# Optimization experiments

Measured on AMD Instinct MI355X. Metric: run time of the kernel, lower is better.

The kernel has to match this reference:

```python
import jax, jax.numpy as jnp
import numpy as np

B, S, D, H = 4, 2048, 1024, 16
DEPTH = D // H


def setup_inputs() -> dict:
    key = jax.random.key(0)
    ks = jax.random.split(key, 12)
    inp = {
        "Q": jax.random.normal(ks[0], (B, S, D), jnp.float32),
        "K": jax.random.normal(ks[1], (B, S, D), jnp.float32),
        "V": jax.random.normal(ks[2], (B, S, D), jnp.float32),
        "mask": jax.random.randint(ks[3], (B, 1, S, S), 0, 2, jnp.int32),
        "Wq": jax.random.normal(ks[4], (D, D), jnp.float32) / np.sqrt(D),
        "bq": jnp.zeros((D,), jnp.float32),
        "Wk": jax.random.normal(ks[5], (D, D), jnp.float32) / np.sqrt(D),
        "bk": jnp.zeros((D,), jnp.float32),
        "Wv": jax.random.normal(ks[6], (D, D), jnp.float32) / np.sqrt(D),
        "bv": jnp.zeros((D,), jnp.float32),
        "Wo": jax.random.normal(ks[7], (D, D), jnp.float32) / np.sqrt(D),
        "bo": jnp.zeros((D,), jnp.float32),
    }
    return inp


def _split_heads(x):
    # (B, S, D) -> (B, H, S, depth)
    b, s, _ = x.shape
    return x.reshape(b, s, H, DEPTH).transpose(0, 2, 1, 3)


def reference(Q, K, V, mask, Wq, bq, Wk, bk, Wv, bv, Wo, bo):
    q = _split_heads(Q @ Wq + bq)  # (B,H,S,d)
    k = _split_heads(K @ Wk + bk)
    v = _split_heads(V @ Wv + bv)
    scores = jnp.einsum("bhqd,bhkd->bhqk", q, k) / jnp.sqrt(jnp.float32(DEPTH))
    m = mask.astype(jnp.bool_).astype(jnp.float32)  # (B,1,S,S)
    scores = scores + (1.0 - m) * -1e9
    attn = jax.nn.softmax(scores, axis=-1)  # (B,H,S,S)
    ctx = jnp.einsum("bhqk,bhkd->bhqd", attn, v)
    ctx = ctx.transpose(0, 2, 1, 3).reshape(Q.shape[0], -1, D)  # (B,S,D)
    out = ctx @ Wo + bo
    return out, attn
```

## Files before the change

kernel.cpp:

```cpp
#include <hip/hip_runtime.h>
#include <hip/hip_bf16.h>

#define B_ 4
#define S_ 2048
#define D_ 1024
#define H_ 16
#define TSZ 8388608L

typedef short short8 __attribute__((ext_vector_type(8)));
typedef float f32x4 __attribute__((ext_vector_type(4)));

__device__ inline unsigned short f2b(float f) {
  __hip_bfloat16 h = __float2bfloat16(f);
  return __builtin_bit_cast(unsigned short, h);
}
__device__ inline void gld16(const unsigned short* g, unsigned short* l) {
  __builtin_amdgcn_global_load_lds(
      (const __attribute__((address_space(1))) void*)g,
      (__attribute__((address_space(3))) void*)l, 16, 0, 0);
}

__global__ __launch_bounds__(256) void mask_pack(const int* __restrict__ mask,
                                                 unsigned int* __restrict__ mp) {
  long t = (long)blockIdx.x * 256 + threadIdx.x;
  const int4* p = (const int4*)(mask + (t >> 4) * (long)S_ + (t & 15) * 128);
  unsigned int w0 = 0, w1 = 0, w2 = 0, w3 = 0;
#pragma unroll
  for (int c = 0; c < 32; c++) {
    int4 v = p[c];
#pragma unroll
    for (int e = 0; e < 4; e++) {
      int k = c * 4 + e;
      int val = e == 0 ? v.x : e == 1 ? v.y : e == 2 ? v.z : v.w;
      int nb = k >> 4, p16 = k & 15;
      int gg = p16 >> 2, r = p16 & 3;
      unsigned bit = ((unsigned)val & 1u) << (nb * 4 + r);
      if (gg == 0) w0 |= bit; else if (gg == 1) w1 |= bit;
      else if (gg == 2) w2 |= bit; else w3 |= bit;
    }
  }
  *(uint4*)(mp + t * 4) = make_uint4(w0, w1, w2, w3);
}

__global__ __launch_bounds__(256) void cvt3(
    const float* __restrict__ Q, const float* __restrict__ K,
    const float* __restrict__ V, unsigned short* __restrict__ qo,
    unsigned short* __restrict__ ko, unsigned short* __restrict__ vo) {
  int seg = blockIdx.x >> 12;
  long i = ((long)(blockIdx.x & 4095) * 256 + threadIdx.x) * 8;
  const float* in = seg == 0 ? Q : seg == 1 ? K : V;
  unsigned short* out = seg == 0 ? qo : seg == 1 ? ko : vo;
  float4 a = *(const float4*)(in + i);
  float4 b = *(const float4*)(in + i + 4);
  short8 u;
  u[0] = (short)f2b(a.x); u[1] = (short)f2b(a.y);
  u[2] = (short)f2b(a.z); u[3] = (short)f2b(a.w);
  u[4] = (short)f2b(b.x); u[5] = (short)f2b(b.y);
  u[6] = (short)f2b(b.z); u[7] = (short)f2b(b.w);
  *(short8*)(out + i) = u;
}

__global__ __launch_bounds__(256) void transpose_w4(
    const float* __restrict__ W0, const float* __restrict__ W1,
    const float* __restrict__ W2, const float* __restrict__ W3,
    unsigned short* __restrict__ T0, unsigned short* __restrict__ T1,
    unsigned short* __restrict__ T2, unsigned short* __restrict__ T3) {
  __shared__ unsigned short t[64 * 72];
  const int z = blockIdx.z;
  const float* W = z == 0 ? W0 : z == 1 ? W1 : z == 2 ? W2 : W3;
  unsigned short* Wt = z == 0 ? T0 : z == 1 ? T1 : z == 2 ? T2 : T3;
  const int tid = threadIdx.x;
  const int k0 = blockIdx.x * 64, n0 = blockIdx.y * 64;
#pragma unroll
  for (int p = 0; p < 4; p++) {
    int e = (p * 256 + tid) * 4;
    int r = e >> 6, c = e & 63;
    float4 v = *(const float4*)(W + (long)(k0 + r) * D_ + n0 + c);
    ushort4 u;
    u.x = f2b(v.x); u.y = f2b(v.y); u.z = f2b(v.z); u.w = f2b(v.w);
    *(ushort4*)(&t[r * 72 + c]) = u;
  }
  __syncthreads();
#pragma unroll
  for (int p = 0; p < 2; p++) {
    int e = (p * 256 + tid) * 8;
    int n = e >> 6, kc = e & 63;
    short8 x;
#pragma unroll
    for (int i = 0; i < 8; i++) x[i] = (short)t[(kc + i) * 72 + n];
    *(short8*)(Wt + (long)(n0 + n) * D_ + k0 + kc) = x;
  }
}

__global__ __launch_bounds__(256) void qkv_gemm(
    const unsigned short* __restrict__ qa, const unsigned short* __restrict__ ka,
    const unsigned short* __restrict__ va, const unsigned short* __restrict__ wq,
    const unsigned short* __restrict__ wk, const unsigned short* __restrict__ wv,
    const float* __restrict__ bqp, const float* __restrict__ bkp,
    const float* __restrict__ bvp, unsigned short* __restrict__ qo,
    unsigned short* __restrict__ ko, unsigned short* __restrict__ vo) {
  __shared__ unsigned short Asm[128 * 32];
  __shared__ unsigned short Bsm[128 * 32];
  const int z = blockIdx.z;
  const unsigned short* A = z == 0 ? qa : z == 1 ? ka : va;
  const unsigned short* Wt = z == 0 ? wq : z == 1 ? wk : wv;
  const float* bias = z == 0 ? bqp : z == 1 ? bkp : bvp;
  unsigned short* outp = z == 0 ? qo : z == 1 ? ko : vo;
  const int tid = threadIdx.x;
  const int lane = tid & 63, wid = tid >> 6;
  const int g = lane >> 4, li = lane & 15;
  const int wm = wid >> 1, wn = wid & 1;
  const long bm = (long)blockIdx.x * 128;
  const long bn = (long)blockIdx.y * 128;

  f32x4 acc[4][4];
#pragma unroll
  for (int i = 0; i < 4; i++)
#pragma unroll
    for (int j = 0; j < 4; j++) acc[i][j] = (f32x4){0.f, 0.f, 0.f, 0.f};

  for (int kt = 0; kt < 32; ++kt) {
    const int k0 = kt * 32;
    __syncthreads();
#pragma unroll
    for (int p = 0; p < 2; p++) {
      int ci = p * 256 + wid * 64 + lane;
      int r = ci >> 2, c = (ci & 3) * 8;
      gld16(A + (bm + r) * 1024L + k0 + c, &Asm[(p * 256 + wid * 64) * 8]);
      gld16(Wt + (bn + r) * 1024L + k0 + c, &Bsm[(p * 256 + wid * 64) * 8]);
    }
    __syncthreads();
    short8 af[4], bf[4];
#pragma unroll
    for (int i = 0; i < 4; i++)
      af[i] = *(const short8*)(&Asm[(wm * 64 + i * 16 + li) * 32 + g * 8]);
#pragma unroll
    for (int i = 0; i < 4; i++)
      bf[i] = *(const short8*)(&Bsm[(wn * 64 + i * 16 + li) * 32 + g * 8]);
#pragma unroll
    for (int i = 0; i < 4; i++)
#pragma unroll
      for (int j = 0; j < 4; j++)
        acc[i][j] =
            __builtin_amdgcn_mfma_f32_16x16x32_bf16(af[i], bf[j], acc[i][j], 0, 0, 0);
  }

#pragma unroll
  for (int i = 0; i < 4; i++) {
    int row0 = (int)bm + wm * 64 + i * 16 + g * 4;
#pragma unroll
    for (int j = 0; j < 4; j++) {
      int col = (int)bn + wn * 64 + j * 16 + li;
      float bvv = bias[col];
      if (z == 2) {
        int b = row0 >> 11, s0 = row0 & 2047;
        int h = col >> 6, dd = col & 63;
        ushort4 u;
#pragma unroll
        for (int jj = 0; jj < 4; jj++) u[jj] = f2b(acc[i][j][jj] + bvv);
        *(ushort4*)(outp + ((long)(b * H_ + h) * 64 + dd) * S_ + s0) = u;
      } else {
#pragma unroll
        for (int jj = 0; jj < 4; jj++) {
          int row = row0 + jj;
          int b = row >> 11, s = row & 2047;
          int h = col >> 6, dd = col & 63;
          outp[(((long)(b * H_ + h)) * S_ + s) * 64 + dd] =
              f2b(acc[i][j][jj] + bvv);
        }
      }
    }
  }
}

__global__ __launch_bounds__(256) void wo_gemm(
    const unsigned short* __restrict__ A, const unsigned short* __restrict__ Wt,
    const float* __restrict__ bias, float* __restrict__ out) {
  __shared__ unsigned short Asm[128 * 32];
  __shared__ unsigned short Bsm[128 * 32];
  const int tid = threadIdx.x;
  const int lane = tid & 63, wid = tid >> 6;
  const int g = lane >> 4, li = lane & 15;
  const int wm = wid >> 1, wn = wid & 1;
  const long bm = (long)blockIdx.x * 128;
  const long bn = (long)blockIdx.y * 128;

  f32x4 acc[4][4];
#pragma unroll
  for (int i = 0; i < 4; i++)
#pragma unroll
    for (int j = 0; j < 4; j++) acc[i][j] = (f32x4){0.f, 0.f, 0.f, 0.f};

  for (int kt = 0; kt < 32; ++kt) {
    const int k0 = kt * 32;
    __syncthreads();
#pragma unroll
    for (int p = 0; p < 2; p++) {
      int ci = p * 256 + wid * 64 + lane;
      int r = ci >> 2, c = (ci & 3) * 8;
      gld16(A + (bm + r) * 1024L + k0 + c, &Asm[(p * 256 + wid * 64) * 8]);
      gld16(Wt + (bn + r) * 1024L + k0 + c, &Bsm[(p * 256 + wid * 64) * 8]);
    }
    __syncthreads();
    short8 af[4], bf[4];
#pragma unroll
    for (int i = 0; i < 4; i++)
      af[i] = *(const short8*)(&Asm[(wm * 64 + i * 16 + li) * 32 + g * 8]);
#pragma unroll
    for (int i = 0; i < 4; i++)
      bf[i] = *(const short8*)(&Bsm[(wn * 64 + i * 16 + li) * 32 + g * 8]);
#pragma unroll
    for (int i = 0; i < 4; i++)
#pragma unroll
      for (int j = 0; j < 4; j++)
        acc[i][j] =
            __builtin_amdgcn_mfma_f32_16x16x32_bf16(af[i], bf[j], acc[i][j], 0, 0, 0);
  }

#pragma unroll
  for (int i = 0; i < 4; i++) {
    int row0 = (int)bm + wm * 64 + i * 16 + g * 4;
#pragma unroll
    for (int j = 0; j < 4; j++) {
      int col = (int)bn + wn * 64 + j * 16 + li;
      float bvv = bias[col];
#pragma unroll
      for (int jj = 0; jj < 4; jj++)
        out[(long)(row0 + jj) * 1024 + col] = acc[i][j][jj] + bvv;
    }
  }
}

__global__ __launch_bounds__(256, 4) void attn_kernel(
    const unsigned short* __restrict__ q,
    const unsigned short* __restrict__ k,
    const unsigned short* __restrict__ vt,
    const unsigned int* __restrict__ mpk,
    float* __restrict__ attn,
    unsigned short* __restrict__ ctx) {
  __shared__ unsigned short k_lds[128 * 72];
  __shared__ unsigned short vt_lds[64 * 136];
  const int tid = threadIdx.x;
  const int lane = tid & 63, wid = tid >> 6;
  const int g = lane >> 4, li = lane & 15;
  const int p0 = blockIdx.x + 32 * blockIdx.y;
  const int xcd = p0 & 7, q8 = p0 >> 3;
  const int bx = q8 & 31;
  const int bh = xcd * 8 + (q8 >> 5);
  const int b = bh >> 4, h = bh & 15;
  const int qw = bx * 64 + wid * 16;
  const int qs = qw + li;

  const unsigned short* qp = q + ((long)bh * S_ + qw) * 64;
  const short8 aq0 = *(const short8*)(qp + li * 64 + g * 8);
  const short8 aq1 = *(const short8*)(qp + li * 64 + 32 + g * 8);
  const unsigned int* mp = mpk + (((long)b * S_ + qs) * 16) * 4 + g;

  const unsigned short* kbase = k + (long)bh * S_ * 64;
  const unsigned short* vbase = vt + (long)bh * 64 * S_;
  int kst[4], kgo[4], vst[4], vgo[4];
#pragma unroll
  for (int p = 0; p < 4; p++) {
    int e = (p * 256 + tid) * 8;
    int krr = e >> 6, kcc = e & 63;
    kst[p] = krr * 72 + kcc;
    kgo[p] = krr * 64 + kcc;
    int vrr = e >> 7, vcc = e & 127;
    int c0 = ((vcc >> 5) << 5) + ((vcc & 8) << 1) + ((vcc & 16) >> 2);
    vst[p] = vrr * 136 + c0;
    vgo[p] = vrr * S_ + vcc;
  }

  float lsum = 0.f;
  short8 kreg[4];
#pragma unroll
  for (int p = 0; p < 4; p++)
    kreg[p] = *(const short8*)(kbase + kgo[p]);
  unsigned int mb_n = mp[0];
  for (int kt = 0; kt < 16; ++kt) {
    __syncthreads();
#pragma unroll
    for (int p = 0; p < 4; p++)
      *(short8*)(&k_lds[kst[p]]) = kreg[p];
    unsigned int mb = mb_n;
    if (kt < 15) {
#pragma unroll
      for (int p = 0; p < 4; p++)
        kreg[p] = *(const short8*)(kbase + (kt + 1) * 8192 + kgo[p]);
      mb_n = mp[(kt + 1) * 4];
    }
    __syncthreads();
#pragma unroll
    for (int nb = 0; nb < 8; nb++) {
      short8 b0 = *(const short8*)(&k_lds[(nb * 16 + li) * 72 + g * 8]);
      short8 b1 = *(const short8*)(&k_lds[(nb * 16 + li) * 72 + 32 + g * 8]);
      f32x4 s = (f32x4){0.f, 0.f, 0.f, 0.f};
      __builtin_amdgcn_s_setprio(1);
      s = __builtin_amdgcn_mfma_f32_16x16x32_bf16(b0, aq0, s, 0, 0, 0);
      s = __builtin_amdgcn_mfma_f32_16x16x32_bf16(b1, aq1, s, 0, 0, 0);
      __builtin_amdgcn_s_setprio(0);
#pragma unroll
      for (int r = 0; r < 4; r++) {
        float sc = s[r] * 0.125f + (((mb >> (nb * 4 + r)) & 1u) ? 0.f : -1e9f);
        lsum += __expf(sc);
      }
    }
  }
  lsum += __shfl_xor(lsum, 16);
  lsum += __shfl_xor(lsum, 32);
  const float linv = (lsum > 0.f) ? 1.0f / lsum : 0.f;

  f32x4 c[4];
#pragma unroll
  for (int i = 0; i < 4; i++) c[i] = (f32x4){0.f, 0.f, 0.f, 0.f};

  short8 vreg[4];
#pragma unroll
  for (int p = 0; p < 4; p++) {
    kreg[p] = *(const short8*)(kbase + kgo[p]);
    vreg[p] = *(const short8*)(vbase + vgo[p]);
  }
  mb_n = mp[0];
  for (int kt = 0; kt < 16; ++kt) {
    __syncthreads();
#pragma unroll
    for (int p = 0; p < 4; p++) {
      *(short8*)(&k_lds[kst[p]]) = kreg[p];
      ushort4* vh = (ushort4*)&vreg[p];
      *(ushort4*)(&vt_lds[vst[p]]) = vh[0];
      *(ushort4*)(&vt_lds[vst[p] + 8]) = vh[1];
    }
    unsigned int mb = mb_n;
    if (kt < 15) {
#pragma unroll
      for (int p = 0; p < 4; p++) {
        kreg[p] = *(const short8*)(kbase + (kt + 1) * 8192 + kgo[p]);
        vreg[p] = *(const short8*)(vbase + (kt + 1) * 128 + vgo[p]);
      }
      mb_n = mp[(kt + 1) * 4];
    }
    __syncthreads();
    float* arow = attn + ((long)bh * S_ + qs) * S_ + kt * 128;
    short8 pu2[4];
#pragma unroll
    for (int nb = 0; nb < 8; nb++) {
      short8 b0 = *(const short8*)(&k_lds[(nb * 16 + li) * 72 + g * 8]);
      short8 b1 = *(const short8*)(&k_lds[(nb * 16 + li) * 72 + 32 + g * 8]);
      f32x4 s = (f32x4){0.f, 0.f, 0.f, 0.f};
      __builtin_amdgcn_s_setprio(1);
      s = __builtin_amdgcn_mfma_f32_16x16x32_bf16(b0, aq0, s, 0, 0, 0);
      s = __builtin_amdgcn_mfma_f32_16x16x32_bf16(b1, aq1, s, 0, 0, 0);
      __builtin_amdgcn_s_setprio(0);
      f32x4 pf;
      ushort4 pu;
#pragma unroll
      for (int r = 0; r < 4; r++) {
        float sc = s[r] * 0.125f + (((mb >> (nb * 4 + r)) & 1u) ? 0.f : -1e9f);
        float pv = __expf(sc) * linv;
        pf[r] = pv;
        pu[r] = f2b(pv);
      }
      __builtin_nontemporal_store(pf, (f32x4*)(arow + nb * 16 + g * 4));
      ((ushort4*)&pu2[nb >> 1])[nb & 1] = pu;
    }
    __builtin_amdgcn_s_setprio(1);
#pragma unroll
    for (int kc = 0; kc < 4; kc++) {
      short8 ap = pu2[kc];
#pragma unroll
      for (int nb2 = 0; nb2 < 4; nb2++) {
        short8 bv =
            *(const short8*)(&vt_lds[(nb2 * 16 + li) * 136 + kc * 32 + g * 8]);
        c[nb2] = __builtin_amdgcn_mfma_f32_16x16x32_bf16(ap, bv, c[nb2], 0, 0, 0);
      }
    }
    __builtin_amdgcn_s_setprio(0);
  }

#pragma unroll
  for (int nb2 = 0; nb2 < 4; nb2++) {
#pragma unroll
    for (int j = 0; j < 4; j++) {
      int qrow = qw + g * 4 + j;
      ctx[((long)(b * S_ + qrow)) * D_ + h * 64 + nb2 * 16 + li] = f2b(c[nb2][j]);
    }
  }
}

extern "C" void kernel_launch(void* const* d_in, const int* in_sizes, int n_in,
                              void* d_out, int out_size, void* d_ws, size_t ws_size,
                              hipStream_t stream) {
  const float* Q = (const float*)d_in[0];
  const float* K = (const float*)d_in[1];
  const float* V = (const float*)d_in[2];
  const int* mask = (const int*)d_in[3];
  const float* Wq = (const float*)d_in[4];
  const float* bq = (const float*)d_in[5];
  const float* Wk = (const float*)d_in[6];
  const float* bk = (const float*)d_in[7];
  const float* Wv = (const float*)d_in[8];
  const float* bv = (const float*)d_in[9];
  const float* Wo = (const float*)d_in[10];
  const float* bo = (const float*)d_in[11];

  float* out = (float*)d_out;
  float* attn = out + TSZ;
  unsigned int* mpack = (unsigned int*)d_out;

  unsigned short* ws = (unsigned short*)d_ws;
  unsigned short* qh = ws;
  unsigned short* kh = ws + TSZ;
  unsigned short* vt = ws + 2 * TSZ;
  unsigned short* ctx = ws + 3 * TSZ;
  unsigned short* qbf = ws + 4 * TSZ;
  unsigned short* kbf = ws + 5 * TSZ;
  unsigned short* vbf = ws + 6 * TSZ;
  unsigned short* wtq = ws + 7 * TSZ;
  unsigned short* wtk = wtq + 1048576;
  unsigned short* wtv = wtk + 1048576;
  unsigned short* wto = wtv + 1048576;

  dim3 bb(256);
  mask_pack<<<512, bb, 0, stream>>>(mask, mpack);
  cvt3<<<12288, bb, 0, stream>>>(Q, K, V, qbf, kbf, vbf);
  transpose_w4<<<dim3(16, 16, 4), bb, 0, stream>>>(Wq, Wk, Wv, Wo, wtq, wtk,
                                                   wtv, wto);
  qkv_gemm<<<dim3(64, 8, 3), bb, 0, stream>>>(qbf, kbf, vbf, wtq, wtk, wtv, bq,
                                              bk, bv, qh, kh, vt);
  attn_kernel<<<dim3(32, 64), bb, 0, stream>>>(qh, kh, vt, mpack, attn, ctx);
  wo_gemm<<<dim3(64, 8), bb, 0, stream>>>(ctx, wto, bo, out);
}
```

Before: 476.7 us.

## Fold softmax scale into Q projection, use exp2, merge prep kernels

The 1/sqrt(depth)·log2(e) factor is applied to Q in the QKV GEMM epilogue. The attention kernel can then call exp2f directly on the raw scores, and masked positions are zeroed by a select instead of adding -1e9 before the exponential. The three preprocessing kernels (mask packing, input bf16 conversion, weight transpose) are merged into one launch that dispatches on block index, saving launch gaps. The risks are small rounding differences from scaling Q before bf16 conversion, and fully masked rows now giving zeros instead of a uniform distribution.

```diff
diff --git a/kernel.cpp b/kernel.cpp
--- a/kernel.cpp
+++ b/kernel.cpp
@@ -6,6 +6,7 @@
 #define D_ 1024
 #define H_ 16
 #define TSZ 8388608L
+#define QSCALE 0.18033688f
 
 typedef short short8 __attribute__((ext_vector_type(8)));
 typedef float f32x4 __attribute__((ext_vector_type(4)));
@@ -20,75 +21,74 @@
       (__attribute__((address_space(3))) void*)l, 16, 0, 0);
 }
 
-__global__ __launch_bounds__(256) void mask_pack(const int* __restrict__ mask,
-                                                 unsigned int* __restrict__ mp) {
-  long t = (long)blockIdx.x * 256 + threadIdx.x;
-  const int4* p = (const int4*)(mask + (t >> 4) * (long)S_ + (t & 15) * 128);
-  unsigned int w0 = 0, w1 = 0, w2 = 0, w3 = 0;
-#pragma unroll
-  for (int c = 0; c < 32; c++) {
-    int4 v = p[c];
-#pragma unroll
-    for (int e = 0; e < 4; e++) {
-      int k = c * 4 + e;
-      int val = e == 0 ? v.x : e == 1 ? v.y : e == 2 ? v.z : v.w;
-      int nb = k >> 4, p16 = k & 15;
-      int gg = p16 >> 2, r = p16 & 3;
-      unsigned bit = ((unsigned)val & 1u) << (nb * 4 + r);
-      if (gg == 0) w0 |= bit; else if (gg == 1) w1 |= bit;
-      else if (gg == 2) w2 |= bit; else w3 |= bit;
-    }
-  }
-  *(uint4*)(mp + t * 4) = make_uint4(w0, w1, w2, w3);
-}
-
-__global__ __launch_bounds__(256) void cvt3(
+__global__ __launch_bounds__(256) void prep_all(
     const float* __restrict__ Q, const float* __restrict__ K,
-    const float* __restrict__ V, unsigned short* __restrict__ qo,
-    unsigned short* __restrict__ ko, unsigned short* __restrict__ vo) {
-  int seg = blockIdx.x >> 12;
-  long i = ((long)(blockIdx.x & 4095) * 256 + threadIdx.x) * 8;
-  const float* in = seg == 0 ? Q : seg == 1 ? K : V;
-  unsigned short* out = seg == 0 ? qo : seg == 1 ? ko : vo;
-  float4 a = *(const float4*)(in + i);
-  float4 b = *(const float4*)(in + i + 4);
-  short8 u;
-  u[0] = (short)f2b(a.x); u[1] = (short)f2b(a.y);
-  u[2] = (short)f2b(a.z); u[3] = (short)f2b(a.w);
-  u[4] = (short)f2b(b.x); u[5] = (short)f2b(b.y);
-  u[6] = (short)f2b(b.z); u[7] = (short)f2b(b.w);
-  *(short8*)(out + i) = u;
-}
-
-__global__ __launch_bounds__(256) void transpose_w4(
+    const float* __restrict__ V, const int* __restrict__ mask,
     const float* __restrict__ W0, const float* __restrict__ W1,
     const float* __restrict__ W2, const float* __restrict__ W3,
+    unsigned short* __restrict__ qo, unsigned short* __restrict__ ko,
+    unsigned short* __restrict__ vo, unsigned int* __restrict__ mp,
     unsigned short* __restrict__ T0, unsigned short* __restrict__ T1,
     unsigned short* __restrict__ T2, unsigned short* __restrict__ T3) {
   __shared__ unsigned short t[64 * 72];
-  const int z = blockIdx.z;
-  const float* W = z == 0 ? W0 : z == 1 ? W1 : z == 2 ? W2 : W3;
-  unsigned short* Wt = z == 0 ? T0 : z == 1 ? T1 : z == 2 ? T2 : T3;
   const int tid = threadIdx.x;
-  const int k0 = blockIdx.x * 64, n0 = blockIdx.y * 64;
-#pragma unroll
-  for (int p = 0; p < 4; p++) {
-    int e = (p * 256 + tid) * 4;
-    int r = e >> 6, c = e & 63;
-    float4 v = *(const float4*)(W + (long)(k0 + r) * D_ + n0 + c);
-    ushort4 u;
-    u.x = f2b(v.x); u.y = f2b(v.y); u.z = f2b(v.z); u.w = f2b(v.w);
-    *(ushort4*)(&t[r * 72 + c]) = u;
-  }
-  __syncthreads();
-#pragma unroll
-  for (int p = 0; p < 2; p++) {
-    int e = (p * 256 + tid) * 8;
-    int n = e >> 6, kc = e & 63;
-    short8 x;
-#pragma unroll
-    for (int i = 0; i < 8; i++) x[i] = (short)t[(kc + i) * 72 + n];
-    *(short8*)(Wt + (long)(n0 + n) * D_ + k0 + kc) = x;
+  if (blockIdx.x < 12288) {
+    int seg = blockIdx.x >> 12;
+    long i = ((long)(blockIdx.x & 4095) * 256 + tid) * 8;
+    const float* in = seg == 0 ? Q : seg == 1 ? K : V;
+    unsigned short* out = seg == 0 ? qo : seg == 1 ? ko : vo;
+    float4 a = *(const float4*)(in + i);
+    float4 b = *(const float4*)(in + i + 4);
+    short8 u;
+    u[0] = (short)f2b(a.x); u[1] = (short)f2b(a.y);
+    u[2] = (short)f2b(a.z); u[3] = (short)f2b(a.w);
+    u[4] = (short)f2b(b.x); u[5] = (short)f2b(b.y);
+    u[6] = (short)f2b(b.z); u[7] = (short)f2b(b.w);
+    *(short8*)(out + i) = u;
+  } else if (blockIdx.x < 12800) {
+    long tt = (long)(blockIdx.x - 12288) * 256 + tid;
+    const int4* p = (const int4*)(mask + (tt >> 4) * (long)S_ + (tt & 15) * 128);
+    unsigned int w0 = 0, w1 = 0, w2 = 0, w3 = 0;
+#pragma unroll
+    for (int c = 0; c < 32; c++) {
+      int4 v = p[c];
+#pragma unroll
+      for (int e = 0; e < 4; e++) {
+        int k = c * 4 + e;
+        int val = e == 0 ? v.x : e == 1 ? v.y : e == 2 ? v.z : v.w;
+        int nb = k >> 4, p16 = k & 15;
+        int gg = p16 >> 2, r = p16 & 3;
+        unsigned bit = ((unsigned)val & 1u) << (nb * 4 + r);
+        if (gg == 0) w0 |= bit; else if (gg == 1) w1 |= bit;
+        else if (gg == 2) w2 |= bit; else w3 |= bit;
+      }
+    }
+    *(uint4*)(mp + tt * 4) = make_uint4(w0, w1, w2, w3);
+  } else {
+    int tz = blockIdx.x - 12800;
+    int z = tz >> 8, rem = tz & 255;
+    const float* W = z == 0 ? W0 : z == 1 ? W1 : z == 2 ? W2 : W3;
+    unsigned short* Wt = z == 0 ? T0 : z == 1 ? T1 : z == 2 ? T2 : T3;
+    const int k0 = (rem >> 4) * 64, n0 = (rem & 15) * 64;
+#pragma unroll
+    for (int p = 0; p < 4; p++) {
+      int e = (p * 256 + tid) * 4;
+      int r = e >> 6, c = e & 63;
+      float4 v = *(const float4*)(W + (long)(k0 + r) * D_ + n0 + c);
+      ushort4 u;
+      u.x = f2b(v.x); u.y = f2b(v.y); u.z = f2b(v.z); u.w = f2b(v.w);
+      *(ushort4*)(&t[r * 72 + c]) = u;
+    }
+    __syncthreads();
+#pragma unroll
+    for (int p = 0; p < 2; p++) {
+      int e = (p * 256 + tid) * 8;
+      int n = e >> 6, kc = e & 63;
+      short8 x;
+#pragma unroll
+      for (int i = 0; i < 8; i++) x[i] = (short)t[(kc + i) * 72 + n];
+      *(short8*)(Wt + (long)(n0 + n) * D_ + k0 + kc) = x;
+    }
   }
 }
 
@@ -106,6 +106,7 @@
   const unsigned short* Wt = z == 0 ? wq : z == 1 ? wk : wv;
   const float* bias = z == 0 ? bqp : z == 1 ? bkp : bvp;
   unsigned short* outp = z == 0 ? qo : z == 1 ? ko : vo;
+  const float osc = (z == 0) ? QSCALE : 1.0f;
   const int tid = threadIdx.x;
   const int lane = tid & 63, wid = tid >> 6;
   const int g = lane >> 4, li = lane & 15;
@@ -166,7 +167,7 @@
           int b = row >> 11, s = row & 2047;
           int h = col >> 6, dd = col & 63;
           outp[(((long)(b * H_ + h)) * S_ + s) * 64 + dd] =
-              f2b(acc[i][j][jj] + bvv);
+              f2b((acc[i][j][jj] + bvv) * osc);
         }
       }
     }
@@ -286,7 +287,7 @@
     if (kt < 15) {
 #pragma unroll
       for (int p = 0; p < 4; p++)
-        kreg[p] = *(const short8*)(kbase + (kt + 1) * 8192 + kgo[p]);
+        kreg[p] = *(const short8*)(kbase + ((long)(kt + 1) * 128) * 64 + kgo[p]);
       mb_n = mp[(kt + 1) * 4];
     }
     __syncthreads();
@@ -301,8 +302,8 @@
       __builtin_amdgcn_s_setprio(0);
 #pragma unroll
       for (int r = 0; r < 4; r++) {
-        float sc = s[r] * 0.125f + (((mb >> (nb * 4 + r)) & 1u) ? 0.f : -1e9f);
-        lsum += __expf(sc);
+        float ev = exp2f(s[r]);
+        lsum += (((mb >> (nb * 4 + r)) & 1u) ? ev : 0.f);
       }
     }
   }
@@ -334,7 +335,7 @@
     if (kt < 15) {
 #pragma unroll
       for (int p = 0; p < 4; p++) {
-        kreg[p] = *(const short8*)(kbase + (kt + 1) * 8192 + kgo[p]);
+        kreg[p] = *(const short8*)(kbase + ((long)(kt + 1) * 128) * 64 + kgo[p]);
         vreg[p] = *(const short8*)(vbase + (kt + 1) * 128 + vgo[p]);
       }
       mb_n = mp[(kt + 1) * 4];
@@ -355,8 +356,8 @@
       ushort4 pu;
 #pragma unroll
       for (int r = 0; r < 4; r++) {
-        float sc = s[r] * 0.125f + (((mb >> (nb * 4 + r)) & 1u) ? 0.f : -1e9f);
-        float pv = __expf(sc) * linv;
+        float ev = exp2f(s[r]) * linv;
+        float pv = (((mb >> (nb * 4 + r)) & 1u) ? ev : 0.f);
         pf[r] = pv;
         pu[r] = f2b(pv);
       }
@@ -421,10 +422,8 @@
   unsigned short* wto = wtv + 1048576;
 
   dim3 bb(256);
-  mask_pack<<<512, bb, 0, stream>>>(mask, mpack);
-  cvt3<<<12288, bb, 0, stream>>>(Q, K, V, qbf, kbf, vbf);
-  transpose_w4<<<dim3(16, 16, 4), bb, 0, stream>>>(Wq, Wk, Wv, Wo, wtq, wtk,
-                                                   wtv, wto);
+  prep_all<<<13824, bb, 0, stream>>>(Q, K, V, mask, Wq, Wk, Wv, Wo, qbf, kbf,
+                                     vbf, mpack, wtq, wtk, wtv, wto);
   qkv_gemm<<<dim3(64, 8, 3), bb, 0, stream>>>(qbf, kbf, vbf, wtq, wtk, wtv, bq,
                                               bk, bv, qh, kh, vt);
   attn_kernel<<<dim3(32, 64), bb, 0, stream>>>(qh, kh, vt, mpack, attn, ctx);
```

Result: slower. 505.6 us (+6.1%).
